# Optimization experiments

Measured on AMD Instinct MI355X. Metric: run time of the kernel, lower is better.

## Reference

```python
import jax, jax.numpy as jnp
import numpy as np

_BLOCK = 32          # _QUANTIZATION_BLOCK_SIZE
_UPPER = 8           # upper_bound = 2**(4-1)-1 + 1 for Q4_0 (bitwidth=4)
_QMAX = 15.0         # 2**bitwidth - 1


def _q4_0_dequant(kernel):
    """Vectorized Q4_0 fake-quantization over 32-element blocks (last axis, no transpose)."""
    orig_dtype = kernel.dtype
    nb = kernel.size // _BLOCK
    blocks = kernel.reshape(nb, _BLOCK).astype(jnp.float32)  # [nb, 32]
    # signed value at the abs-argmax position of each block
    amax_idx = jnp.argmax(jnp.abs(blocks), axis=1)
    max_val = jnp.take_along_axis(blocks, amax_idx[:, None], axis=1)  # [nb, 1]
    d = -max_val / _UPPER
    safe_d = jnp.where(d == 0.0, 1.0, d)
    safe_inv_d = jnp.where(d == 0.0, 0.0, 1.0 / safe_d)
    scale = d.astype(jnp.float16).astype(jnp.float32)  # fp16 scale round-trip
    qs = jnp.clip(jnp.trunc(blocks * safe_inv_d + (_UPPER + 0.5)), 0.0, _QMAX)
    deq = scale * (qs - _UPPER)
    return deq.reshape(kernel.shape).astype(orig_dtype)


def _ste_q4_0(kernel):
    """Straight-through estimator wrapper (identity gradient)."""
    zero = kernel - jax.lax.stop_gradient(kernel)
    return zero + jax.lax.stop_gradient(_q4_0_dequant(kernel))


def setup_inputs() -> dict:
    key = jax.random.key(0)
    k1, k2, k3 = jax.random.split(key, 3)
    d_in, features = 8192, 8192
    inputs = jax.random.normal(k1, (1, 32, d_in), dtype=jnp.float32)
    kernel = jax.random.normal(k2, (d_in, features), dtype=jnp.float32) * 0.02
    bias = jax.random.normal(k3, (features,), dtype=jnp.float32) * 0.02
    return {"inputs": inputs, "kernel": kernel, "bias": bias}


def reference(inputs, kernel, bias):
    w = _ste_q4_0(kernel)                      # fake-quantized weight [d_in, features]
    y = inputs @ w                             # [B, S, features]
    y = y + bias
    return y
```

## Files before the change

kernel.cpp:

```cpp
#include <hip/hip_runtime.h>
#include <hip/hip_fp16.h>

#define MDIM 32
#define KDIM 8192
#define NDIM 8192
#define NT 128
#define KC 512
#define BK 64
#define NTILES (KC / BK)
#define NSPLIT (KDIM / KC)
#define LSTR 130

typedef __fp16 half8 __attribute__((ext_vector_type(8)));
typedef float f32x4 __attribute__((ext_vector_type(4)));

__device__ __forceinline__ unsigned pk_u32(float a, float b) {
#if __has_builtin(__builtin_amdgcn_cvt_pkrtz)
  return __builtin_bit_cast(unsigned, __builtin_amdgcn_cvt_pkrtz(a, b));
#else
  __fp16 r2[2] = {(__fp16)a, (__fp16)b};
  return __builtin_bit_cast(unsigned, r2);
#endif
}

__global__ __launch_bounds__(256) void xpack_kernel(const float* __restrict__ x,
                                                    uint4* __restrict__ xpf) {
  const int T  = blockIdx.x * 256 + threadIdx.x;
  const int sg = T >> 7;
  const int r  = T & 127;
  const int mt = r >> 6;
  const int L  = r & 63;
  const int m  = mt * 16 + (L & 15);
  const int k  = sg * 32 + (L >> 4) * 8;
  const float4* p = reinterpret_cast<const float4*>(x + (size_t)m * KDIM + k);
  float4 u0 = p[0], u1 = p[1];
  uint4 o;
  o.x = pk_u32(u0.x, u0.y);
  o.y = pk_u32(u0.z, u0.w);
  o.z = pk_u32(u1.x, u1.y);
  o.w = pk_u32(u1.z, u1.w);
  xpf[T] = o;
}

__global__ __launch_bounds__(256, 4) void fused_q4_gemm(
    const uint4* __restrict__ xpf,
    const float* __restrict__ w,
    const float* __restrict__ bias,
    float* __restrict__ out)
{
  __shared__ unsigned sW[32 * LSTR];

  const int t    = threadIdx.x;
  const int n0   = blockIdx.x * NT;
  const int k0   = blockIdx.y * KC;
  const int lane = t & 63;
  const int wv   = t >> 6;
  const int l15  = lane & 15;
  const int q    = lane >> 4;
  const int h    = lane >> 5;
  const int nl   = (lane & 31) * 4;

  f32x4 acc00 = {0.f, 0.f, 0.f, 0.f};
  f32x4 acc01 = {0.f, 0.f, 0.f, 0.f};
  f32x4 acc10 = {0.f, 0.f, 0.f, 0.f};
  f32x4 acc11 = {0.f, 0.f, 0.f, 0.f};

  float4 V[8];

#pragma unroll
  for (int p = 0; p < 8; ++p) {
    const int sp = p * 4 + wv;
    V[p] = *reinterpret_cast<const float4*>(
        w + (size_t)(k0 + 2 * sp + h) * NDIM + n0 + nl);
  }

  for (int tt = 0; tt < NTILES; ++tt) {
    const int kt = k0 + tt * BK;

#pragma unroll
    for (int p = 0; p < 8; ++p) {
      const int sp = p * 4 + wv;
      float4 v = V[p];
      float ba = -1.0f, bv = 0.0f, a;
      a = fabsf(v.x); if (a > ba) { ba = a; bv = v.x; }
      a = fabsf(v.y); if (a > ba) { ba = a; bv = v.y; }
      a = fabsf(v.z); if (a > ba) { ba = a; bv = v.z; }
      a = fabsf(v.w); if (a > ba) { ba = a; bv = v.w; }
#pragma unroll
      for (int msk = 1; msk <= 4; msk <<= 1) {
        float pa = __shfl_xor(ba, msk);
        float pv = __shfl_xor(bv, msk);
        if (pa > ba) { ba = pa; bv = pv; }
      }
      float d   = bv * -0.125f;
      float inv = (d == 0.0f) ? 0.0f : 1.0f / d;
      float s   = __half2float(__float2half(d));
      float q0f = fminf(fmaxf(truncf(fmaf(v.x, inv, 8.5f)), 0.0f), 15.0f);
      float q1f = fminf(fmaxf(truncf(fmaf(v.y, inv, 8.5f)), 0.0f), 15.0f);
      float q2f = fminf(fmaxf(truncf(fmaf(v.z, inv, 8.5f)), 0.0f), 15.0f);
      float q3f = fminf(fmaxf(truncf(fmaf(v.w, inv, 8.5f)), 0.0f), 15.0f);
      unsigned A = pk_u32((q0f - 8.0f) * s, (q1f - 8.0f) * s);
      unsigned B = pk_u32((q2f - 8.0f) * s, (q3f - 8.0f) * s);
      unsigned pA = (unsigned)__shfl_xor((int)A, 32);
      unsigned pB = (unsigned)__shfl_xor((int)B, 32);
      unsigned lo0 = h ? pA : A, hi0 = h ? A : pA;
      unsigned lo1 = h ? pB : B, hi1 = h ? B : pB;
      unsigned D0 = (lo0 & 0xffffu) | (hi0 << 16);
      unsigned D1 = (lo0 >> 16)     | (hi0 & 0xffff0000u);
      unsigned D2 = (lo1 & 0xffffu) | (hi1 << 16);
      unsigned D3 = (lo1 >> 16)     | (hi1 & 0xffff0000u);
      uint2 wr = h ? make_uint2(D2, D3) : make_uint2(D0, D1);
      *reinterpret_cast<uint2*>(&sW[sp * LSTR + nl + 2 * h]) = wr;
    }

    __syncthreads();

    if (tt + 1 < NTILES) {
#pragma unroll
      for (int p = 0; p < 8; ++p) {
        const int sp = p * 4 + wv;
        V[p] = *reinterpret_cast<const float4*>(
            w + (size_t)(kt + BK + 2 * sp + h) * NDIM + n0 + nl);
      }
    }

    const int sg0 = kt >> 5;
#pragma unroll
    for (int ks = 0; ks < 2; ++ks) {
      const uint4* ap = xpf + ((size_t)(sg0 + ks) * 2) * 64 + lane;
      uint4 a0u = ap[0];
      uint4 a1u = ap[64];
      const int kpb = ks * 16 + q * 4;
      const int nA = wv * 32 + l15;
      const int nB = nA + 16;
      uint4 b0u, b1u;
      b0u.x = sW[(kpb + 0) * LSTR + nA];
      b0u.y = sW[(kpb + 1) * LSTR + nA];
      b0u.z = sW[(kpb + 2) * LSTR + nA];
      b0u.w = sW[(kpb + 3) * LSTR + nA];
      b1u.x = sW[(kpb + 0) * LSTR + nB];
      b1u.y = sW[(kpb + 1) * LSTR + nB];
      b1u.z = sW[(kpb + 2) * LSTR + nB];
      b1u.w = sW[(kpb + 3) * LSTR + nB];
      half8 a0 = __builtin_bit_cast(half8, a0u);
      half8 a1 = __builtin_bit_cast(half8, a1u);
      half8 b0 = __builtin_bit_cast(half8, b0u);
      half8 b1 = __builtin_bit_cast(half8, b1u);
      acc00 = __builtin_amdgcn_mfma_f32_16x16x32_f16(a0, b0, acc00, 0, 0, 0);
      acc01 = __builtin_amdgcn_mfma_f32_16x16x32_f16(a0, b1, acc01, 0, 0, 0);
      acc10 = __builtin_amdgcn_mfma_f32_16x16x32_f16(a1, b0, acc10, 0, 0, 0);
      acc11 = __builtin_amdgcn_mfma_f32_16x16x32_f16(a1, b1, acc11, 0, 0, 0);
    }

    __syncthreads();
  }

  const int gn0 = n0 + wv * 32 + l15;
  const int gn1 = gn0 + 16;
  const float bv0 = (blockIdx.y == 0) ? bias[gn0] : 0.0f;
  const float bv1 = (blockIdx.y == 0) ? bias[gn1] : 0.0f;
#pragma unroll
  for (int r = 0; r < 4; ++r) {
    const int m0 = q * 4 + r;
    const int m1 = m0 + 16;
    atomicAdd(out + (size_t)m0 * NDIM + gn0, acc00[r] + bv0);
    atomicAdd(out + (size_t)m0 * NDIM + gn1, acc01[r] + bv1);
    atomicAdd(out + (size_t)m1 * NDIM + gn0, acc10[r] + bv0);
    atomicAdd(out + (size_t)m1 * NDIM + gn1, acc11[r] + bv1);
  }
}

extern "C" void kernel_launch(void* const* d_in, const int* in_sizes, int n_in,
                              void* d_out, int out_size, void* d_ws, size_t ws_size,
                              hipStream_t stream) {
  const float* x    = (const float*)d_in[0];
  const float* w    = (const float*)d_in[1];
  const float* bias = (const float*)d_in[2];
  float* out  = (float*)d_out;
  uint4* xpf  = (uint4*)d_ws;

  (void)hipMemsetAsync(out, 0, (size_t)MDIM * NDIM * sizeof(float), stream);
  xpack_kernel<<<128, 256, 0, stream>>>(x, xpf);

  dim3 grid(NDIM / NT, NSPLIT);
  fused_q4_gemm<<<grid, 256, 0, stream>>>(xpf, w, bias, out);
}
```

Before: 362.4 us.

## Give each wave a private LDS tile and drop block-wide barriers

Each wave now loads, quantizes and stores only the 32 columns it consumes, into its own LDS region, so both __syncthreads per tile are gone. The thread mapping changes so a lane pair covers one 32-element quantization block across two k-rows. That replaces the three-step shuffle argmax with a rotated-bit unsigned max and one shuffle, and removes the cross-half packing shuffles. Activation fragments are now loaded at the top of each tile. Correctness relies on wave-level lockstep between the LDS writes and reads with no explicit barrier, and on the rotate trick matching argmax tie-breaking on |x|.

```diff
diff --git a/kernel.cpp b/kernel.cpp
--- a/kernel.cpp
+++ b/kernel.cpp
@@ -9,7 +9,7 @@
 #define BK 64
 #define NTILES (KC / BK)
 #define NSPLIT (KDIM / KC)
-#define LSTR 130
+#define LSTRW 36
 
 typedef __fp16 half8 __attribute__((ext_vector_type(8)));
 typedef float f32x4 __attribute__((ext_vector_type(4)));
@@ -21,6 +21,17 @@
   __fp16 r2[2] = {(__fp16)a, (__fp16)b};
   return __builtin_bit_cast(unsigned, r2);
 #endif
+}
+
+__device__ __forceinline__ unsigned rotk(float x) {
+  unsigned u = __builtin_bit_cast(unsigned, x);
+  return (u << 1) | (u >> 31);
+}
+__device__ __forceinline__ unsigned umaxu(unsigned a, unsigned b) { return a > b ? a : b; }
+
+__device__ __forceinline__ float dq1(float v, float inv, float s) {
+  float qf = fminf(fmaxf(truncf(fmaf(v, inv, 8.5f)), 0.0f), 15.0f);
+  return (qf - 8.0f) * s;
 }
 
 __global__ __launch_bounds__(256) void xpack_kernel(const float* __restrict__ x,
@@ -48,102 +59,96 @@
     const float* __restrict__ bias,
     float* __restrict__ out)
 {
-  __shared__ unsigned sW[32 * LSTR];
+  __shared__ unsigned sW[4 * 32 * LSTRW];
 
-  const int t    = threadIdx.x;
+  const int tid  = threadIdx.x;
   const int n0   = blockIdx.x * NT;
   const int k0   = blockIdx.y * KC;
-  const int lane = t & 63;
-  const int wv   = t >> 6;
+  const int lane = tid & 63;
+  const int wv   = tid >> 6;
   const int l15  = lane & 15;
   const int q    = lane >> 4;
-  const int h    = lane >> 5;
-  const int nl   = (lane & 31) * 4;
+  const int kp   = lane >> 1;
+  const int h    = lane & 1;
+
+  unsigned* __restrict__ sWv = sW + wv * (32 * LSTRW);
 
   f32x4 acc00 = {0.f, 0.f, 0.f, 0.f};
   f32x4 acc01 = {0.f, 0.f, 0.f, 0.f};
   f32x4 acc10 = {0.f, 0.f, 0.f, 0.f};
   f32x4 acc11 = {0.f, 0.f, 0.f, 0.f};
 
+  const int gc0 = n0 + wv * 32 + 16 * h;
+  const float* wp = w + (size_t)(k0 + 2 * kp) * NDIM + gc0;
+  const uint4* ap = xpf + (size_t)(k0 >> 5) * 128 + lane;
+
   float4 V[8];
-
-#pragma unroll
-  for (int p = 0; p < 8; ++p) {
-    const int sp = p * 4 + wv;
-    V[p] = *reinterpret_cast<const float4*>(
-        w + (size_t)(k0 + 2 * sp + h) * NDIM + n0 + nl);
+  {
+    const float4* p0 = reinterpret_cast<const float4*>(wp);
+    const float4* p1 = reinterpret_cast<const float4*>(wp + NDIM);
+    V[0] = p0[0]; V[1] = p0[1]; V[2] = p0[2]; V[3] = p0[3];
+    V[4] = p1[0]; V[5] = p1[1]; V[6] = p1[2]; V[7] = p1[3];
   }
 
   for (int tt = 0; tt < NTILES; ++tt) {
-    const int kt = k0 + tt * BK;
+    uint4 xa0[2], xa1[2];
+    xa0[0] = ap[0];   xa1[0] = ap[64];
+    xa0[1] = ap[128]; xa1[1] = ap[192];
+    ap += 256;
+
+    unsigned pe = 0u, po = 0u;
+#pragma unroll
+    for (int i = 0; i < 4; ++i) {
+      pe = umaxu(pe, rotk(V[i].x));     pe = umaxu(pe, rotk(V[i].y));
+      pe = umaxu(pe, rotk(V[i].z));     pe = umaxu(pe, rotk(V[i].w));
+      po = umaxu(po, rotk(V[i + 4].x)); po = umaxu(po, rotk(V[i + 4].y));
+      po = umaxu(po, rotk(V[i + 4].z)); po = umaxu(po, rotk(V[i + 4].w));
+    }
+    pe = umaxu(pe, (unsigned)__shfl_xor((int)pe, 1));
+    po = umaxu(po, (unsigned)__shfl_xor((int)po, 1));
+    const float bve = __builtin_bit_cast(float, (pe >> 1) | (pe << 31));
+    const float bvo = __builtin_bit_cast(float, (po >> 1) | (po << 31));
+    const float de = bve * -0.125f;
+    const float dd = bvo * -0.125f;
+    const float ie = (de == 0.0f) ? 0.0f : 1.0f / de;
+    const float io = (dd == 0.0f) ? 0.0f : 1.0f / dd;
+    const float se = __half2float(__float2half(de));
+    const float so = __half2float(__float2half(dd));
+
+    uint4 P[4];
+#pragma unroll
+    for (int i = 0; i < 4; ++i) {
+      P[i].x = pk_u32(dq1(V[i].x, ie, se), dq1(V[i + 4].x, io, so));
+      P[i].y = pk_u32(dq1(V[i].y, ie, se), dq1(V[i + 4].y, io, so));
+      P[i].z = pk_u32(dq1(V[i].z, ie, se), dq1(V[i + 4].z, io, so));
+      P[i].w = pk_u32(dq1(V[i].w, ie, se), dq1(V[i + 4].w, io, so));
+    }
+
+    if (tt + 1 < NTILES) {
+      wp += (size_t)BK * NDIM;
+      const float4* p0 = reinterpret_cast<const float4*>(wp);
+      const float4* p1 = reinterpret_cast<const float4*>(wp + NDIM);
+      V[0] = p0[0]; V[1] = p0[1]; V[2] = p0[2]; V[3] = p0[3];
+      V[4] = p1[0]; V[5] = p1[1]; V[6] = p1[2]; V[7] = p1[3];
+    }
+
+    uint4* wb = reinterpret_cast<uint4*>(sWv + kp * LSTRW + 16 * h);
+    wb[0] = P[0]; wb[1] = P[1]; wb[2] = P[2]; wb[3] = P[3];
 
 #pragma unroll
-    for (int p = 0; p < 8; ++p) {
-      const int sp = p * 4 + wv;
-      float4 v = V[p];
-      float ba = -1.0f, bv = 0.0f, a;
-      a = fabsf(v.x); if (a > ba) { ba = a; bv = v.x; }
-      a = fabsf(v.y); if (a > ba) { ba = a; bv = v.y; }
-      a = fabsf(v.z); if (a > ba) { ba = a; bv = v.z; }
-      a = fabsf(v.w); if (a > ba) { ba = a; bv = v.w; }
-#pragma unroll
-      for (int msk = 1; msk <= 4; msk <<= 1) {
-        float pa = __shfl_xor(ba, msk);
-        float pv = __shfl_xor(bv, msk);
-        if (pa > ba) { ba = pa; bv = pv; }
-      }
-      float d   = bv * -0.125f;
-      float inv = (d == 0.0f) ? 0.0f : 1.0f / d;
-      float s   = __half2float(__float2half(d));
-      float q0f = fminf(fmaxf(truncf(fmaf(v.x, inv, 8.5f)), 0.0f), 15.0f);
-      float q1f = fminf(fmaxf(truncf(fmaf(v.y, inv, 8.5f)), 0.0f), 15.0f);
-      float q2f = fminf(fmaxf(truncf(fmaf(v.z, inv, 8.5f)), 0.0f), 15.0f);
-      float q3f = fminf(fmaxf(truncf(fmaf(v.w, inv, 8.5f)), 0.0f), 15.0f);
-      unsigned A = pk_u32((q0f - 8.0f) * s, (q1f - 8.0f) * s);
-      unsigned B = pk_u32((q2f - 8.0f) * s, (q3f - 8.0f) * s);
-      unsigned pA = (unsigned)__shfl_xor((int)A, 32);
-      unsigned pB = (unsigned)__shfl_xor((int)B, 32);
-      unsigned lo0 = h ? pA : A, hi0 = h ? A : pA;
-      unsigned lo1 = h ? pB : B, hi1 = h ? B : pB;
-      unsigned D0 = (lo0 & 0xffffu) | (hi0 << 16);
-      unsigned D1 = (lo0 >> 16)     | (hi0 & 0xffff0000u);
-      unsigned D2 = (lo1 & 0xffffu) | (hi1 << 16);
-      unsigned D3 = (lo1 >> 16)     | (hi1 & 0xffff0000u);
-      uint2 wr = h ? make_uint2(D2, D3) : make_uint2(D0, D1);
-      *reinterpret_cast<uint2*>(&sW[sp * LSTR + nl + 2 * h]) = wr;
-    }
-
-    __syncthreads();
-
-    if (tt + 1 < NTILES) {
-#pragma unroll
-      for (int p = 0; p < 8; ++p) {
-        const int sp = p * 4 + wv;
-        V[p] = *reinterpret_cast<const float4*>(
-            w + (size_t)(kt + BK + 2 * sp + h) * NDIM + n0 + nl);
-      }
-    }
-
-    const int sg0 = kt >> 5;
-#pragma unroll
     for (int ks = 0; ks < 2; ++ks) {
-      const uint4* ap = xpf + ((size_t)(sg0 + ks) * 2) * 64 + lane;
-      uint4 a0u = ap[0];
-      uint4 a1u = ap[64];
       const int kpb = ks * 16 + q * 4;
-      const int nA = wv * 32 + l15;
-      const int nB = nA + 16;
       uint4 b0u, b1u;
-      b0u.x = sW[(kpb + 0) * LSTR + nA];
-      b0u.y = sW[(kpb + 1) * LSTR + nA];
-      b0u.z = sW[(kpb + 2) * LSTR + nA];
-      b0u.w = sW[(kpb + 3) * LSTR + nA];
-      b1u.x = sW[(kpb + 0) * LSTR + nB];
-      b1u.y = sW[(kpb + 1) * LSTR + nB];
-      b1u.z = sW[(kpb + 2) * LSTR + nB];
-      b1u.w = sW[(kpb + 3) * LSTR + nB];
-      half8 a0 = __builtin_bit_cast(half8, a0u);
-      half8 a1 = __builtin_bit_cast(half8, a1u);
+      b0u.x = sWv[(kpb + 0) * LSTRW + l15];
+      b0u.y = sWv[(kpb + 1) * LSTRW + l15];
+      b0u.z = sWv[(kpb + 2) * LSTRW + l15];
+      b0u.w = sWv[(kpb + 3) * LSTRW + l15];
+      b1u.x = sWv[(kpb + 0) * LSTRW + 16 + l15];
+      b1u.y = sWv[(kpb + 1) * LSTRW + 16 + l15];
+      b1u.z = sWv[(kpb + 2) * LSTRW + 16 + l15];
+      b1u.w = sWv[(kpb + 3) * LSTRW + 16 + l15];
+      half8 a0 = __builtin_bit_cast(half8, xa0[ks]);
+      half8 a1 = __builtin_bit_cast(half8, xa1[ks]);
       half8 b0 = __builtin_bit_cast(half8, b0u);
       half8 b1 = __builtin_bit_cast(half8, b1u);
       acc00 = __builtin_amdgcn_mfma_f32_16x16x32_f16(a0, b0, acc00, 0, 0, 0);
@@ -151,8 +156,6 @@
       acc10 = __builtin_amdgcn_mfma_f32_16x16x32_f16(a1, b0, acc10, 0, 0, 0);
       acc11 = __builtin_amdgcn_mfma_f32_16x16x32_f16(a1, b1, acc11, 0, 0, 0);
     }
-
-    __syncthreads();
   }
 
   const int gn0 = n0 + wv * 32 + l15;
```

Measured after the change: 369.7 us. About the same (+2.0%).
